# Optimization experiments

Measured on AMD Instinct MI355X. Metric: run time of the kernel, lower is better.

## Reference

```python
import jax, jax.numpy as jnp
import numpy as np

B, T, N = 128, 256, 128   # batch, input suffix (query positions), bunch size
ATTN_DIM, VEC_DIM = 512, 512
NEG_INF = -1e30


def setup_inputs() -> dict:
    key = jax.random.key(0)
    k1, k2, k3, k4, k5, k6, k7 = jax.random.split(key, 7)
    inputs = jax.random.normal(k1, (B, T, VEC_DIM), dtype=jnp.float32)
    attend_over = jax.random.normal(k2, (B, N, ATTN_DIM), dtype=jnp.float32)
    attend_mask = jax.random.randint(k3, (B, N), 0, 2) > 0
    # kaiming-uniform-ish init for bi_weight (fan_in = vec_dim)
    bound = float(np.sqrt(1.0 / VEC_DIM))
    bi_weight = jax.random.uniform(k4, (ATTN_DIM, VEC_DIM), minval=-bound, maxval=bound, dtype=jnp.float32)
    a_w = jax.random.uniform(k5, (ATTN_DIM,), minval=-bound, maxval=bound, dtype=jnp.float32)
    b_w = jax.random.uniform(k6, (VEC_DIM,), minval=-bound, maxval=bound, dtype=jnp.float32)
    bias = jax.random.uniform(k7, (1,), minval=-bound, maxval=bound, dtype=jnp.float32)
    return {"inputs": inputs, "attend_over": attend_over, "attend_mask": attend_mask,
            "bi_weight": bi_weight, "a_w": a_w, "b_w": b_w, "bias": bias}


def reference(inputs, attend_over, attend_mask, bi_weight, a_w, b_w, bias):
    # bilinear score: a^T M b  -> (B, T, N)
    aM = jnp.einsum('bna,av->bnv', attend_over, bi_weight)          # (B, N, VEC)
    sim = jnp.einsum('btv,bnv->btn', inputs, aM)                    # (B, T, N)
    # linear terms: w_a^T a  and  w_b^T b
    lin_a = jnp.einsum('bna,a->bn', attend_over, a_w)               # (B, N)
    lin_b = jnp.einsum('btv,v->bt', inputs, b_w)                    # (B, T)
    sim = sim + lin_a[:, None, :] + lin_b[:, :, None] + bias[0]
    sim = jnp.tanh(sim)
    # masked softmax over the bunch dim N
    masked = jnp.where(attend_mask[:, None, :], sim, NEG_INF)
    attn = jax.nn.softmax(masked, axis=-1)                          # (B, T, N)
    attn = attn * attend_mask[:, None, :].astype(attn.dtype)
    # weighted sum of attended vectors -> context (B, T, ATTN_DIM)
    context = jnp.einsum('btn,bna->bta', attn, attend_over)
    return context
```

## Files before the change

### kernel.cpp

```cpp
#include <hip/hip_runtime.h>

#define Bsz 128
#define Tsz 256
#define Nsz 128
#define Asz 512
#define Vsz 512
#define PAD 40
#define LIN_BLOCKS 12288

typedef __attribute__((ext_vector_type(8))) short bh8;
typedef __attribute__((ext_vector_type(8))) unsigned short us8;
typedef __attribute__((ext_vector_type(4))) float f32x4;

__device__ __forceinline__ unsigned short f2bf(float x) {
  unsigned int u = __float_as_uint(x);
  return (unsigned short)((u + 0x7fffu + ((u >> 16) & 1u)) >> 16);
}
__device__ __forceinline__ float bf2f(unsigned short h) {
  return __uint_as_float(((unsigned int)h) << 16);
}
__device__ __forceinline__ float fast_tanh(float x) {
  float ax = fabsf(x);
  float e = __expf(-2.f * ax);
  float t = (1.f - e) / (1.f + e);
  return copysignf(t, x);
}

__global__ __launch_bounds__(256) void prep(
    const float* __restrict__ AO, const float* __restrict__ inputs,
    const float* __restrict__ W, const float* __restrict__ a_w,
    const float* __restrict__ b_w, float* __restrict__ lin_a,
    float* __restrict__ lin_b, unsigned short* __restrict__ WT_hi,
    unsigned short* __restrict__ WT_lo)
{
  __shared__ float t[64][65];
  int tid = threadIdx.x;
  if (blockIdx.x < LIN_BLOCKS) {
    int gw = (blockIdx.x * 256 + tid) >> 6;
    int lane = tid & 63;
    const float* src; const float* w; float* dst;
    if (gw < Bsz * Nsz) { src = AO + (long)gw * Asz; w = a_w; dst = lin_a + gw; }
    else { int r = gw - Bsz * Nsz; src = inputs + (long)r * Vsz; w = b_w; dst = lin_b + r; }
    float4 x0 = *(const float4*)(src + lane * 4);
    float4 x1 = *(const float4*)(src + 256 + lane * 4);
    float4 w0 = *(const float4*)(w + lane * 4);
    float4 w1 = *(const float4*)(w + 256 + lane * 4);
    float d = x0.x*w0.x + x0.y*w0.y + x0.z*w0.z + x0.w*w0.w
            + x1.x*w1.x + x1.y*w1.y + x1.z*w1.z + x1.w*w1.w;
#pragma unroll
    for (int off = 32; off; off >>= 1) d += __shfl_xor(d, off);
    if (lane == 0) *dst = d;
  } else {
    int bb = blockIdx.x - LIN_BLOCKS;
    int a0 = (bb & 7) * 64, v0 = (bb >> 3) * 64;
#pragma unroll
    for (int l = 0; l < 4; ++l) {
      int idx = tid + l * 256;
      int r = idx >> 4, c = (idx & 15) * 4;
      float4 v = *(const float4*)(W + (long)(a0 + r) * Vsz + v0 + c);
      t[r][c] = v.x; t[r][c+1] = v.y; t[r][c+2] = v.z; t[r][c+3] = v.w;
    }
    __syncthreads();
#pragma unroll
    for (int l = 0; l < 4; ++l) {
      int idx = tid + l * 256;
      int r = idx >> 4, c = (idx & 15) * 4;
      ushort4 h, lo;
      unsigned short* hp = (unsigned short*)&h;
      unsigned short* lp = (unsigned short*)&lo;
#pragma unroll
      for (int j = 0; j < 4; ++j) {
        float x = t[c + j][r];
        hp[j] = f2bf(x);
        lp[j] = f2bf(x - bf2f(hp[j]));
      }
      *(ushort4*)&WT_hi[(long)(v0 + r) * Asz + a0 + c] = h;
      *(ushort4*)&WT_lo[(long)(v0 + r) * Asz + a0 + c] = lo;
    }
  }
}

__global__ __launch_bounds__(256) void gemm_aM(
    const float* __restrict__ AO, const unsigned short* __restrict__ WT_hi,
    const unsigned short* __restrict__ WT_lo, unsigned int* __restrict__ aMp)
{
  int m0 = blockIdx.x * 128, n0 = blockIdx.y * 128;
  __shared__ unsigned short a_hi[128][PAD], a_lo[128][PAD];
  __shared__ unsigned short b_hi[128][PAD], b_lo[128][PAD];
  int tid = threadIdx.x;
  int wave = tid >> 6, lane = tid & 63;
  int wr = wave >> 1, wc = wave & 1;
  int lr = lane & 15, kg = lane >> 4;
  f32x4 acc[4][4] = {};
  for (int k0 = 0; k0 < Asz; k0 += 32) {
#pragma unroll
    for (int l = 0; l < 4; ++l) {
      int idx = tid + l * 256;
      int r = idx >> 3, c = (idx & 7) * 4;
      float4 v = *(const float4*)(AO + (long)(m0 + r) * Asz + k0 + c);
      float vv[4] = {v.x, v.y, v.z, v.w};
      ushort4 h, lo;
      unsigned short* hp = (unsigned short*)&h;
      unsigned short* lp = (unsigned short*)&lo;
#pragma unroll
      for (int j = 0; j < 4; ++j) {
        hp[j] = f2bf(vv[j]);
        lp[j] = f2bf(vv[j] - bf2f(hp[j]));
      }
      *(ushort4*)&a_hi[r][c] = h;
      *(ushort4*)&a_lo[r][c] = lo;
    }
#pragma unroll
    for (int l = 0; l < 2; ++l) {
      int idx = tid + l * 256;
      int r = idx >> 2, c = (idx & 3) * 8;
      *(us8*)&b_hi[r][c] = *(const us8*)&WT_hi[(long)(n0 + r) * Asz + k0 + c];
      *(us8*)&b_lo[r][c] = *(const us8*)&WT_lo[(long)(n0 + r) * Asz + k0 + c];
    }
    __syncthreads();
    bh8 ah[4], bh_[4], al[4], bl[4];
#pragma unroll
    for (int m = 0; m < 4; ++m) {
      ah[m] = *(const bh8*)&a_hi[wr * 64 + m * 16 + lr][kg * 8];
      al[m] = *(const bh8*)&a_lo[wr * 64 + m * 16 + lr][kg * 8];
    }
#pragma unroll
    for (int n = 0; n < 4; ++n) {
      bh_[n] = *(const bh8*)&b_hi[wc * 64 + n * 16 + lr][kg * 8];
      bl[n]  = *(const bh8*)&b_lo[wc * 64 + n * 16 + lr][kg * 8];
    }
#pragma unroll
    for (int m = 0; m < 4; ++m)
#pragma unroll
      for (int n = 0; n < 4; ++n) {
        acc[m][n] = __builtin_amdgcn_mfma_f32_16x16x32_bf16(ah[m], bh_[n], acc[m][n], 0, 0, 0);
        acc[m][n] = __builtin_amdgcn_mfma_f32_16x16x32_bf16(ah[m], bl[n], acc[m][n], 0, 0, 0);
        acc[m][n] = __builtin_amdgcn_mfma_f32_16x16x32_bf16(al[m], bh_[n], acc[m][n], 0, 0, 0);
      }
    __syncthreads();
  }
#pragma unroll
  for (int m = 0; m < 4; ++m)
#pragma unroll
    for (int n = 0; n < 4; ++n)
#pragma unroll
      for (int j = 0; j < 4; ++j) {
        float x = acc[m][n][j];
        unsigned short h = f2bf(x);
        unsigned short l2 = f2bf(x - bf2f(h));
        aMp[(long)(m0 + wr * 64 + m * 16 + kg * 4 + j) * Vsz + n0 + wc * 64 + n * 16 + lr]
          = (unsigned int)h | ((unsigned int)l2 << 16);
      }
}

__global__ __launch_bounds__(512) void sim_fused(
    const float* __restrict__ inputs, const unsigned int* __restrict__ aMp,
    const float* __restrict__ lin_a, const float* __restrict__ lin_b,
    const int* __restrict__ mask, const float* __restrict__ bias,
    unsigned short* __restrict__ attn_bf)
{
  __shared__ union SU {
    struct { unsigned short a_hi[128][PAD], a_lo[128][PAD], b_hi[128][PAD], b_lo[128][PAD]; } st;
    float S[128][132];
  } u;
  int b = blockIdx.y;
  int t0 = blockIdx.x * 128;
  int tid = threadIdx.x;
  int wave = tid >> 6, lane = tid & 63;
  int wr = wave >> 1, wc = wave & 1;
  int lr = lane & 15, kg = lane >> 4;
  const float* Ap = inputs + ((long)b * Tsz + t0) * Vsz;
  const unsigned int* Bp = aMp + (long)b * Nsz * Vsz;
  f32x4 acc[2][4] = {};
  for (int k0 = 0; k0 < Vsz; k0 += 32) {
#pragma unroll
    for (int l = 0; l < 2; ++l) {
      int idx = tid + l * 512;
      int r = idx >> 3, c = (idx & 7) * 4;
      float4 v = *(const float4*)(Ap + (long)r * Vsz + k0 + c);
      float vv[4] = {v.x, v.y, v.z, v.w};
      ushort4 h, lo;
      unsigned short* hp = (unsigned short*)&h;
      unsigned short* lp = (unsigned short*)&lo;
#pragma unroll
      for (int j = 0; j < 4; ++j) {
        hp[j] = f2bf(vv[j]);
        lp[j] = f2bf(vv[j] - bf2f(hp[j]));
      }
      *(ushort4*)&u.st.a_hi[r][c] = h;
      *(ushort4*)&u.st.a_lo[r][c] = lo;
    }
#pragma unroll
    for (int l = 0; l < 2; ++l) {
      int idx = tid + l * 512;
      int r = idx >> 3, c = (idx & 7) * 4;
      uint4 v = *(const uint4*)(Bp + (long)r * Vsz + k0 + c);
      unsigned int vv[4] = {v.x, v.y, v.z, v.w};
      ushort4 h, lo;
      unsigned short* hp = (unsigned short*)&h;
      unsigned short* lp = (unsigned short*)&lo;
#pragma unroll
      for (int j = 0; j < 4; ++j) {
        hp[j] = (unsigned short)(vv[j] & 0xffffu);
        lp[j] = (unsigned short)(vv[j] >> 16);
      }
      *(ushort4*)&u.st.b_hi[r][c] = h;
      *(ushort4*)&u.st.b_lo[r][c] = lo;
    }
    __syncthreads();
    bh8 ah[2], al[2], bh_[4], bl[4];
#pragma unroll
    for (int m = 0; m < 2; ++m) {
      ah[m] = *(const bh8*)&u.st.a_hi[wr * 32 + m * 16 + lr][kg * 8];
      al[m] = *(const bh8*)&u.st.a_lo[wr * 32 + m * 16 + lr][kg * 8];
    }
#pragma unroll
    for (int n = 0; n < 4; ++n) {
      bh_[n] = *(const bh8*)&u.st.b_hi[wc * 64 + n * 16 + lr][kg * 8];
      bl[n]  = *(const bh8*)&u.st.b_lo[wc * 64 + n * 16 + lr][kg * 8];
    }
#pragma unroll
    for (int m = 0; m < 2; ++m)
#pragma unroll
      for (int n = 0; n < 4; ++n) {
        acc[m][n] = __builtin_amdgcn_mfma_f32_16x16x32_bf16(ah[m], bh_[n], acc[m][n], 0, 0, 0);
        acc[m][n] = __builtin_amdgcn_mfma_f32_16x16x32_bf16(ah[m], bl[n], acc[m][n], 0, 0, 0);
        acc[m][n] = __builtin_amdgcn_mfma_f32_16x16x32_bf16(al[m], bh_[n], acc[m][n], 0, 0, 0);
      }
    __syncthreads();
  }
#pragma unroll
  for (int m = 0; m < 2; ++m)
#pragma unroll
    for (int n = 0; n < 4; ++n)
#pragma unroll
      for (int j = 0; j < 4; ++j)
        u.S[wr * 32 + m * 16 + kg * 4 + j][wc * 64 + n * 16 + lr] = acc[m][n][j];
  __syncthreads();

  float la0 = lin_a[b * Nsz + lane];
  float la1 = lin_a[b * Nsz + 64 + lane];
  int   mk0 = mask[b * Nsz + lane];
  int   mk1 = mask[b * Nsz + 64 + lane];
  float bs  = bias[0];
  for (int r8 = 0; r8 < 16; ++r8) {
    int r = wave * 16 + r8;
    int tI = t0 + r;
    float lb = lin_b[b * Tsz + tI] + bs;
    float s0 = u.S[r][lane] + la0 + lb;
    float s1 = u.S[r][64 + lane] + la1 + lb;
    s0 = fast_tanh(s0); s1 = fast_tanh(s1);
    float v0 = mk0 ? s0 : -1e30f;
    float v1 = mk1 ? s1 : -1e30f;
    float mx = fmaxf(v0, v1);
#pragma unroll
    for (int off = 32; off; off >>= 1) mx = fmaxf(mx, __shfl_xor(mx, off));
    float e0 = mk0 ? __expf(v0 - mx) : 0.f;
    float e1 = mk1 ? __expf(v1 - mx) : 0.f;
    float sm = e0 + e1;
#pragma unroll
    for (int off = 32; off; off >>= 1) sm += __shfl_xor(sm, off);
    float inv = 1.f / sm;
    long base = ((long)b * Tsz + tI) * Nsz;
    attn_bf[base + lane]      = f2bf(e0 * inv);
    attn_bf[base + 64 + lane] = f2bf(e1 * inv);
  }
}

__global__ __launch_bounds__(256) void ao_transpose(
    const float* __restrict__ AO, unsigned short* __restrict__ AOt)
{
  __shared__ unsigned short t[128][128];
  int b = blockIdx.x >> 2;
  int a0 = (blockIdx.x & 3) * 128;
  int tid = threadIdx.x;
#pragma unroll
  for (int l = 0; l < 16; ++l) {
    int idx = tid + l * 256;
    int r = idx >> 5, c = (idx & 31) * 4;
    float4 v = *(const float4*)(AO + ((long)b * Nsz + r) * Asz + a0 + c);
    ushort4 h;
    unsigned short* hp = (unsigned short*)&h;
    hp[0] = f2bf(v.x); hp[1] = f2bf(v.y); hp[2] = f2bf(v.z); hp[3] = f2bf(v.w);
    int key = ((r >> 3) & 7) << 2;
    *(ushort4*)&t[r][c ^ key] = h;
  }
  __syncthreads();
#pragma unroll
  for (int l = 0; l < 8; ++l) {
    int idx = tid + l * 256;
    int ra = idx >> 4, cc = idx & 15;
    int key = (cc & 7) << 2;
    us8 g;
#pragma unroll
    for (int j = 0; j < 8; ++j) g[j] = t[cc * 8 + j][ra ^ key];
    *(us8*)&AOt[((long)b * Asz + a0 + ra) * Nsz + cc * 8] = g;
  }
}

__global__ __launch_bounds__(256) void gemm_ctx(
    const unsigned short* __restrict__ attn_bf, const unsigned short* __restrict__ AOt,
    float* __restrict__ out)
{
  int b = blockIdx.z;
  int m0 = blockIdx.x * 128, n0 = blockIdx.y * 128;
  __shared__ unsigned short a_t[128][PAD], b_t[128][PAD];
  int tid = threadIdx.x;
  int wave = tid >> 6, lane = tid & 63;
  int wr = wave >> 1, wc = wave & 1;
  int lr = lane & 15, kg = lane >> 4;
  const unsigned short* Ap = attn_bf + (long)b * Tsz * Nsz;
  const unsigned short* Bp = AOt + (long)b * Asz * Nsz;
  f32x4 acc[4][4] = {};
  for (int k0 = 0; k0 < Nsz; k0 += 32) {
#pragma unroll
    for (int l = 0; l < 2; ++l) {
      int idx = tid + l * 256;
      int r = idx >> 2, c = (idx & 3) * 8;
      *(us8*)&a_t[r][c] = *(const us8*)&Ap[(long)(m0 + r) * Nsz + k0 + c];
      *(us8*)&b_t[r][c] = *(const us8*)&Bp[(long)(n0 + r) * Nsz + k0 + c];
    }
    __syncthreads();
    bh8 af[4], bf_[4];
#pragma unroll
    for (int m = 0; m < 4; ++m) af[m] = *(const bh8*)&a_t[wr * 64 + m * 16 + lr][kg * 8];
#pragma unroll
    for (int n = 0; n < 4; ++n) bf_[n] = *(const bh8*)&b_t[wc * 64 + n * 16 + lr][kg * 8];
#pragma unroll
    for (int m = 0; m < 4; ++m)
#pragma unroll
      for (int n = 0; n < 4; ++n)
        acc[m][n] = __builtin_amdgcn_mfma_f32_16x16x32_bf16(af[m], bf_[n], acc[m][n], 0, 0, 0);
    __syncthreads();
  }
#pragma unroll
  for (int m = 0; m < 4; ++m)
#pragma unroll
    for (int n = 0; n < 4; ++n)
#pragma unroll
      for (int j = 0; j < 4; ++j)
        out[((long)b * Tsz + m0 + wr * 64 + m * 16 + kg * 4 + j) * Asz + n0 + wc * 64 + n * 16 + lr]
          = acc[m][n][j];
}

extern "C" void kernel_launch(void* const* d_in, const int* in_sizes, int n_in,
                              void* d_out, int out_size, void* d_ws, size_t ws_size,
                              hipStream_t stream) {
  const float* inputs = (const float*)d_in[0];
  const float* AO     = (const float*)d_in[1];
  const int*   mask   = (const int*)d_in[2];
  const float* W      = (const float*)d_in[3];
  const float* a_w    = (const float*)d_in[4];
  const float* b_w    = (const float*)d_in[5];
  const float* bias   = (const float*)d_in[6];
  float* out = (float*)d_out;
  char* wsb  = (char*)d_ws;

  unsigned int*   aMp     = (unsigned int*)wsb;
  unsigned short* AOt     = (unsigned short*)wsb;
  unsigned short* WT_hi   = (unsigned short*)(wsb + 33554432);
  unsigned short* WT_lo   = (unsigned short*)(wsb + 34078720);
  float*          lin_a   = (float*)(wsb + 34603008);
  float*          lin_b   = (float*)(wsb + 34668544);
  unsigned short* attn_bf = (unsigned short*)(wsb + 34799616);

  prep<<<LIN_BLOCKS + 64, 256, 0, stream>>>(AO, inputs, W, a_w, b_w, lin_a, lin_b, WT_hi, WT_lo);
  gemm_aM<<<dim3(128, 4), 256, 0, stream>>>(AO, WT_hi, WT_lo, aMp);
  sim_fused<<<dim3(2, 128), 512, 0, stream>>>(inputs, aMp, lin_a, lin_b, mask, bias, attn_bf);
  ao_transpose<<<512, 256, 0, stream>>>(AO, AOt);
  gemm_ctx<<<dim3(2, 4, 128), 256, 0, stream>>>(attn_bf, AOt, out);
}
```

Measured before the change: 258.4 us.

## Use direct global-to-LDS loads, register-split A operands, and smaller sim tiles

Replaces register-staged LDS fills of B operands with global_load_lds 16-byte direct loads into unpadded LDS, and loads the fp32 A operand straight into registers while splitting it into bf16 hi/lo by truncation. aM is now stored as separate hi and lo planes, and sim_fused uses 64-row tiles so the grid holds twice as many blocks. The goal is to cut LDS traffic, VGPR staging and conversion cost, and to raise occupancy. Risks: unpadded LDS may cause bank conflicts, and truncation in place of round-to-nearest changes the numerics slightly.

Measured after the change: 265.6 us. 2.8% more time.

```diff
diff --git a/kernel.cpp b/kernel.cpp
--- a/kernel.cpp
+++ b/kernel.cpp
@@ -5,11 +5,9 @@
 #define Nsz 128
 #define Asz 512
 #define Vsz 512
-#define PAD 40
 #define LIN_BLOCKS 12288
 
 typedef __attribute__((ext_vector_type(8))) short bh8;
-typedef __attribute__((ext_vector_type(8))) unsigned short us8;
 typedef __attribute__((ext_vector_type(4))) float f32x4;
 
 __device__ __forceinline__ unsigned short f2bf(float x) {
@@ -24,6 +22,30 @@
   float e = __expf(-2.f * ax);
   float t = (1.f - e) / (1.f + e);
   return copysignf(t, x);
+}
+
+__device__ __forceinline__ void gld16(const void* g, void* l) {
+  __builtin_amdgcn_global_load_lds(
+      (const __attribute__((address_space(1))) unsigned int*)g,
+      (__attribute__((address_space(3))) unsigned int*)l, 16, 0, 0);
+}
+
+struct Frag2 { bh8 hi, lo; };
+__device__ __forceinline__ Frag2 load_split8(const float* p) {
+  float4 x0 = *(const float4*)p;
+  float4 x1 = *(const float4*)(p + 4);
+  float xs[8] = {x0.x, x0.y, x0.z, x0.w, x1.x, x1.y, x1.z, x1.w};
+  union { unsigned int u[4]; bh8 v; } H, L;
+#pragma unroll
+  for (int i = 0; i < 4; ++i) {
+    unsigned int a = __float_as_uint(xs[2 * i]);
+    unsigned int b = __float_as_uint(xs[2 * i + 1]);
+    H.u[i] = (a >> 16) | (b & 0xffff0000u);
+    float la = xs[2 * i]     - __uint_as_float(a & 0xffff0000u);
+    float lb = xs[2 * i + 1] - __uint_as_float(b & 0xffff0000u);
+    L.u[i] = (__float_as_uint(la) >> 16) | (__float_as_uint(lb) & 0xffff0000u);
+  }
+  Frag2 r; r.hi = H.v; r.lo = L.v; return r;
 }
 
 __global__ __launch_bounds__(256) void prep(
@@ -82,48 +104,34 @@
 
 __global__ __launch_bounds__(256) void gemm_aM(
     const float* __restrict__ AO, const unsigned short* __restrict__ WT_hi,
-    const unsigned short* __restrict__ WT_lo, unsigned int* __restrict__ aMp)
-{
-  int m0 = blockIdx.x * 128, n0 = blockIdx.y * 128;
-  __shared__ unsigned short a_hi[128][PAD], a_lo[128][PAD];
-  __shared__ unsigned short b_hi[128][PAD], b_lo[128][PAD];
+    const unsigned short* __restrict__ WT_lo,
+    unsigned short* __restrict__ aM_hi, unsigned short* __restrict__ aM_lo)
+{
+  __shared__ unsigned short b_hi[128][32];
+  __shared__ unsigned short b_lo[128][32];
   int tid = threadIdx.x;
   int wave = tid >> 6, lane = tid & 63;
   int wr = wave >> 1, wc = wave & 1;
   int lr = lane & 15, kg = lane >> 4;
+  long m0 = (long)blockIdx.x * 128;
+  int  n0 = blockIdx.y * 128;
   f32x4 acc[4][4] = {};
   for (int k0 = 0; k0 < Asz; k0 += 32) {
 #pragma unroll
-    for (int l = 0; l < 4; ++l) {
-      int idx = tid + l * 256;
-      int r = idx >> 3, c = (idx & 7) * 4;
-      float4 v = *(const float4*)(AO + (long)(m0 + r) * Asz + k0 + c);
-      float vv[4] = {v.x, v.y, v.z, v.w};
-      ushort4 h, lo;
-      unsigned short* hp = (unsigned short*)&h;
-      unsigned short* lp = (unsigned short*)&lo;
-#pragma unroll
-      for (int j = 0; j < 4; ++j) {
-        hp[j] = f2bf(vv[j]);
-        lp[j] = f2bf(vv[j] - bf2f(hp[j]));
-      }
-      *(ushort4*)&a_hi[r][c] = h;
-      *(ushort4*)&a_lo[r][c] = lo;
-    }
-#pragma unroll
-    for (int l = 0; l < 2; ++l) {
-      int idx = tid + l * 256;
-      int r = idx >> 2, c = (idx & 3) * 8;
-      *(us8*)&b_hi[r][c] = *(const us8*)&WT_hi[(long)(n0 + r) * Asz + k0 + c];
-      *(us8*)&b_lo[r][c] = *(const us8*)&WT_lo[(long)(n0 + r) * Asz + k0 + c];
-    }
-    __syncthreads();
-    bh8 ah[4], bh_[4], al[4], bl[4];
-#pragma unroll
-    for (int m = 0; m < 4; ++m) {
-      ah[m] = *(const bh8*)&a_hi[wr * 64 + m * 16 + lr][kg * 8];
-      al[m] = *(const bh8*)&a_lo[wr * 64 + m * 16 + lr][kg * 8];
-    }
+    for (int rep = 0; rep < 2; ++rep) {
+      int seg = wave + rep * 4;
+      int i = seg * 64 + lane;
+      int r = i >> 2, c8 = (i & 3) * 8;
+      long off = (long)(n0 + r) * Asz + k0 + c8;
+      gld16(WT_hi + off, (char*)&b_hi[0][0] + seg * 1024);
+      gld16(WT_lo + off, (char*)&b_lo[0][0] + seg * 1024);
+    }
+    Frag2 a[4];
+#pragma unroll
+    for (int m = 0; m < 4; ++m)
+      a[m] = load_split8(AO + (m0 + wr * 64 + m * 16 + lr) * Asz + k0 + kg * 8);
+    __syncthreads();
+    bh8 bh_[4], bl[4];
 #pragma unroll
     for (int n = 0; n < 4; ++n) {
       bh_[n] = *(const bh8*)&b_hi[wc * 64 + n * 16 + lr][kg * 8];
@@ -133,9 +141,9 @@
     for (int m = 0; m < 4; ++m)
 #pragma unroll
       for (int n = 0; n < 4; ++n) {
-        acc[m][n] = __builtin_amdgcn_mfma_f32_16x16x32_bf16(ah[m], bh_[n], acc[m][n], 0, 0, 0);
-        acc[m][n] = __builtin_amdgcn_mfma_f32_16x16x32_bf16(ah[m], bl[n], acc[m][n], 0, 0, 0);
-        acc[m][n] = __builtin_amdgcn_mfma_f32_16x16x32_bf16(al[m], bh_[n], acc[m][n], 0, 0, 0);
+        acc[m][n] = __builtin_amdgcn_mfma_f32_16x16x32_bf16(a[m].hi, bh_[n], acc[m][n], 0, 0, 0);
+        acc[m][n] = __builtin_amdgcn_mfma_f32_16x16x32_bf16(a[m].hi, bl[n],  acc[m][n], 0, 0, 0);
+        acc[m][n] = __builtin_amdgcn_mfma_f32_16x16x32_bf16(a[m].lo, bh_[n], acc[m][n], 0, 0, 0);
       }
     __syncthreads();
   }
@@ -146,96 +154,73 @@
 #pragma unroll
       for (int j = 0; j < 4; ++j) {
         float x = acc[m][n][j];
-        unsigned short h = f2bf(x);
-        unsigned short l2 = f2bf(x - bf2f(h));
-        aMp[(long)(m0 + wr * 64 + m * 16 + kg * 4 + j) * Vsz + n0 + wc * 64 + n * 16 + lr]
-          = (unsigned int)h | ((unsigned int)l2 << 16);
+        unsigned int u = __float_as_uint(x);
+        unsigned short h = (unsigned short)(u >> 16);
+        float lof = x - __uint_as_float(u & 0xffff0000u);
+        unsigned short l = (unsigned short)(__float_as_uint(lof) >> 16);
+        long row = m0 + wr * 64 + m * 16 + kg * 4 + j;
+        int  col = n0 + wc * 64 + n * 16 + lr;
+        aM_hi[row * Asz + col] = h;
+        aM_lo[row * Asz + col] = l;
       }
 }
 
 __global__ __launch_bounds__(512) void sim_fused(
-    const float* __restrict__ inputs, const unsigned int* __restrict__ aMp,
-    const float* __restrict__ lin_a, const float* __restrict__ lin_b,
-    const int* __restrict__ mask, const float* __restrict__ bias,
-    unsigned short* __restrict__ attn_bf)
+    const float* __restrict__ inputs, const unsigned short* __restrict__ aMh,
+    const unsigned short* __restrict__ aMl, const float* __restrict__ lin_a,
+    const float* __restrict__ lin_b, const int* __restrict__ mask,
+    const float* __restrict__ bias, unsigned short* __restrict__ attn_bf)
 {
   __shared__ union SU {
-    struct { unsigned short a_hi[128][PAD], a_lo[128][PAD], b_hi[128][PAD], b_lo[128][PAD]; } st;
-    float S[128][132];
+    struct { unsigned short b_hi[128][32], b_lo[128][32]; } st;
+    float S[64][132];
   } u;
   int b = blockIdx.y;
-  int t0 = blockIdx.x * 128;
+  int t0 = blockIdx.x * 64;
   int tid = threadIdx.x;
   int wave = tid >> 6, lane = tid & 63;
-  int wr = wave >> 1, wc = wave & 1;
+  int wr = wave >> 2, wc = wave & 3;
   int lr = lane & 15, kg = lane >> 4;
   const float* Ap = inputs + ((long)b * Tsz + t0) * Vsz;
-  const unsigned int* Bp = aMp + (long)b * Nsz * Vsz;
-  f32x4 acc[2][4] = {};
+  const unsigned short* Bh = aMh + (long)b * Nsz * Vsz;
+  const unsigned short* Bl = aMl + (long)b * Nsz * Vsz;
+  f32x4 acc[2][2] = {};
   for (int k0 = 0; k0 < Vsz; k0 += 32) {
-#pragma unroll
-    for (int l = 0; l < 2; ++l) {
-      int idx = tid + l * 512;
-      int r = idx >> 3, c = (idx & 7) * 4;
-      float4 v = *(const float4*)(Ap + (long)r * Vsz + k0 + c);
-      float vv[4] = {v.x, v.y, v.z, v.w};
-      ushort4 h, lo;
-      unsigned short* hp = (unsigned short*)&h;
-      unsigned short* lp = (unsigned short*)&lo;
-#pragma unroll
-      for (int j = 0; j < 4; ++j) {
-        hp[j] = f2bf(vv[j]);
-        lp[j] = f2bf(vv[j] - bf2f(hp[j]));
+    {
+      int i = wave * 64 + lane;
+      int r = i >> 2, c8 = (i & 3) * 8;
+      long off = (long)r * Vsz + k0 + c8;
+      gld16(Bh + off, (char*)&u.st.b_hi[0][0] + wave * 1024);
+      gld16(Bl + off, (char*)&u.st.b_lo[0][0] + wave * 1024);
+    }
+    Frag2 a[2];
+#pragma unroll
+    for (int m = 0; m < 2; ++m)
+      a[m] = load_split8(Ap + (long)(wr * 32 + m * 16 + lr) * Vsz + k0 + kg * 8);
+    __syncthreads();
+    bh8 bh_[2], bl[2];
+#pragma unroll
+    for (int n = 0; n < 2; ++n) {
+      bh_[n] = *(const bh8*)&u.st.b_hi[wc * 32 + n * 16 + lr][kg * 8];
+      bl[n]  = *(const bh8*)&u.st.b_lo[wc * 32 + n * 16 + lr][kg * 8];
+    }
+#pragma unroll
+    for (int m = 0; m < 2; ++m)
+#pragma unroll
+      for (int n = 0; n < 2; ++n) {
+        acc[m][n] = __builtin_amdgcn_mfma_f32_16x16x32_bf16(a[m].hi, bh_[n], acc[m][n], 0, 0, 0);
+        acc[m][n] = __builtin_amdgcn_mfma_f32_16x16x32_bf16(a[m].hi, bl[n],  acc[m][n], 0, 0, 0);
+        acc[m][n] = __builtin_amdgcn_mfma_f32_16x16x32_bf16(a[m].lo, bh_[n], acc[m][n], 0, 0, 0);
       }
-      *(ushort4*)&u.st.a_hi[r][c] = h;
-      *(ushort4*)&u.st.a_lo[r][c] = lo;
-    }
-#pragma unroll
-    for (int l = 0; l < 2; ++l) {
-      int idx = tid + l * 512;
-      int r = idx >> 3, c = (idx & 7) * 4;
-      uint4 v = *(const uint4*)(Bp + (long)r * Vsz + k0 + c);
-      unsigned int vv[4] = {v.x, v.y, v.z, v.w};
-      ushort4 h, lo;
-      unsigned short* hp = (unsigned short*)&h;
-      unsigned short* lp = (unsigned short*)&lo;
-#pragma unroll
-      for (int j = 0; j < 4; ++j) {
-        hp[j] = (unsigned short)(vv[j] & 0xffffu);
-        lp[j] = (unsigned short)(vv[j] >> 16);
-      }
-      *(ushort4*)&u.st.b_hi[r][c] = h;
-      *(ushort4*)&u.st.b_lo[r][c] = lo;
-    }
-    __syncthreads();
-    bh8 ah[2], al[2], bh_[4], bl[4];
-#pragma unroll
-    for (int m = 0; m < 2; ++m) {
-      ah[m] = *(const bh8*)&u.st.a_hi[wr * 32 + m * 16 + lr][kg * 8];
-      al[m] = *(const bh8*)&u.st.a_lo[wr * 32 + m * 16 + lr][kg * 8];
-    }
-#pragma unroll
-    for (int n = 0; n < 4; ++n) {
-      bh_[n] = *(const bh8*)&u.st.b_hi[wc * 64 + n * 16 + lr][kg * 8];
-      bl[n]  = *(const bh8*)&u.st.b_lo[wc * 64 + n * 16 + lr][kg * 8];
-    }
-#pragma unroll
-    for (int m = 0; m < 2; ++m)
-#pragma unroll
-      for (int n = 0; n < 4; ++n) {
-        acc[m][n] = __builtin_amdgcn_mfma_f32_16x16x32_bf16(ah[m], bh_[n], acc[m][n], 0, 0, 0);
-        acc[m][n] = __builtin_amdgcn_mfma_f32_16x16x32_bf16(ah[m], bl[n], acc[m][n], 0, 0, 0);
-        acc[m][n] = __builtin_amdgcn_mfma_f32_16x16x32_bf16(al[m], bh_[n], acc[m][n], 0, 0, 0);
-      }
     __syncthreads();
   }
 #pragma unroll
   for (int m = 0; m < 2; ++m)
 #pragma unroll
-    for (int n = 0; n < 4; ++n)
+    for (int n = 0; n < 2; ++n)
 #pragma unroll
       for (int j = 0; j < 4; ++j)
-        u.S[wr * 32 + m * 16 + kg * 4 + j][wc * 64 + n * 16 + lr] = acc[m][n][j];
+        u.S[wr * 32 + m * 16 + kg * 4 + j][wc * 32 + n * 16 + lr] = acc[m][n][j];
   __syncthreads();
 
   float la0 = lin_a[b * Nsz + lane];
@@ -243,8 +228,9 @@
   int   mk0 = mask[b * Nsz + lane];
   int   mk1 = mask[b * Nsz + 64 + lane];
   float bs  = bias[0];
-  for (int r8 = 0; r8 < 16; ++r8) {
-    int r = wave * 16 + r8;
+#pragma unroll
+  for (int rr = 0; rr < 8; ++rr) {
+    int r = wave * 8 + rr;
     int tI = t0 + r;
     float lb = lin_b[b * Tsz + tI] + bs;
     float s0 = u.S[r][lane] + la0 + lb;
@@ -291,10 +277,10 @@
     int idx = tid + l * 256;
     int ra = idx >> 4, cc = idx & 15;
     int key = (cc & 7) << 2;
-    us8 g;
-#pragma unroll
-    for (int j = 0; j < 8; ++j) g[j] = t[cc * 8 + j][ra ^ key];
-    *(us8*)&AOt[((long)b * Asz + a0 + ra) * Nsz + cc * 8] = g;
+    union { unsigned short s[8]; uint4 q; } g;
+#pragma unroll
+    for (int j = 0; j < 8; ++j) g.s[j] = t[cc * 8 + j][ra ^ key];
+    *(uint4*)&AOt[((long)b * Asz + a0 + ra) * Nsz + cc * 8] = g.q;
   }
 }
 
@@ -302,9 +288,10 @@
     const unsigned short* __restrict__ attn_bf, const unsigned short* __restrict__ AOt,
     float* __restrict__ out)
 {
+  __shared__ unsigned short a_t[128][32];
+  __shared__ unsigned short b_t[128][32];
   int b = blockIdx.z;
   int m0 = blockIdx.x * 128, n0 = blockIdx.y * 128;
-  __shared__ unsigned short a_t[128][PAD], b_t[128][PAD];
   int tid = threadIdx.x;
   int wave = tid >> 6, lane = tid & 63;
   int wr = wave >> 1, wc = wave & 1;
@@ -314,11 +301,12 @@
   f32x4 acc[4][4] = {};
   for (int k0 = 0; k0 < Nsz; k0 += 32) {
 #pragma unroll
-    for (int l = 0; l < 2; ++l) {
-      int idx = tid + l * 256;
-      int r = idx >> 2, c = (idx & 3) * 8;
-      *(us8*)&a_t[r][c] = *(const us8*)&Ap[(long)(m0 + r) * Nsz + k0 + c];
-      *(us8*)&b_t[r][c] = *(const us8*)&Bp[(long)(n0 + r) * Nsz + k0 + c];
+    for (int rep = 0; rep < 2; ++rep) {
+      int seg = wave + rep * 4;
+      int i = seg * 64 + lane;
+      int r = i >> 2, c8 = (i & 3) * 8;
+      gld16(Ap + (long)(m0 + r) * Nsz + k0 + c8, (char*)&a_t[0][0] + seg * 1024);
+      gld16(Bp + (long)(n0 + r) * Nsz + k0 + c8, (char*)&b_t[0][0] + seg * 1024);
     }
     __syncthreads();
     bh8 af[4], bf_[4];
@@ -356,7 +344,8 @@
   float* out = (float*)d_out;
   char* wsb  = (char*)d_ws;
 
-  unsigned int*   aMp     = (unsigned int*)wsb;
+  unsigned short* aM_hi   = (unsigned short*)wsb;
+  unsigned short* aM_lo   = (unsigned short*)(wsb + 16777216);
   unsigned short* AOt     = (unsigned short*)wsb;
   unsigned short* WT_hi   = (unsigned short*)(wsb + 33554432);
   unsigned short* WT_lo   = (unsigned short*)(wsb + 34078720);
@@ -365,8 +354,8 @@
   unsigned short* attn_bf = (unsigned short*)(wsb + 34799616);
 
   prep<<<LIN_BLOCKS + 64, 256, 0, stream>>>(AO, inputs, W, a_w, b_w, lin_a, lin_b, WT_hi, WT_lo);
-  gemm_aM<<<dim3(128, 4), 256, 0, stream>>>(AO, WT_hi, WT_lo, aMp);
-  sim_fused<<<dim3(2, 128), 512, 0, stream>>>(inputs, aMp, lin_a, lin_b, mask, bias, attn_bf);
+  gemm_aM<<<dim3(128, 4), 256, 0, stream>>>(AO, WT_hi, WT_lo, aM_hi, aM_lo);
+  sim_fused<<<dim3(4, 128), 512, 0, stream>>>(inputs, aM_hi, aM_lo, lin_a, lin_b, mask, bias, attn_bf);
   ao_transpose<<<512, 256, 0, stream>>>(AO, AOt);
   gemm_ctx<<<dim3(2, 4, 128), 256, 0, stream>>>(attn_bf, AOt, out);
 }
```
